# Performance work log

Measured on AMD Instinct MI355X. Metric: run time of the kernel, lower is better.

Reference implementation:

```python
import jax, jax.numpy as jnp
import numpy as np

# Standard SMPL kinematic tree (parent of each of the 24 joints)
PARENTS = np.array([-1, 0, 0, 0, 1, 2, 3, 4, 5, 6, 7, 8, 9, 9, 9, 12, 13, 14, 16, 17, 18, 19, 20, 21])
B, V, NJ = 512, 6890, 24


def rodrigues(r):
    # r: (N,3) axis-angle -> (N,3,3) rotation matrices
    theta = jnp.linalg.norm(r, axis=1, keepdims=True) + 1e-8  # (N,1), eps mirrors the noise trick in torch code
    rh = r / theta                                            # (N,3) unit axis
    x, y, z = rh[:, 0], rh[:, 1], rh[:, 2]
    zero = jnp.zeros_like(x)
    K = jnp.stack([zero, -z, y, z, zero, -x, -y, x, zero], axis=1).reshape(-1, 3, 3)
    cos = jnp.cos(theta)[:, :, None]
    sin = jnp.sin(theta)[:, :, None]
    outer = rh[:, :, None] * rh[:, None, :]
    I3 = jnp.eye(3, dtype=r.dtype)
    return cos * I3 + (1.0 - cos) * outer + sin * K


def _make_A(Ri, ti):
    # Ri: (B,3,3), ti: (B,3) -> homogeneous (B,4,4)
    Rt = jnp.concatenate([Ri, ti[:, :, None]], axis=2)  # (B,3,4)
    bottom = jnp.broadcast_to(jnp.array([0.0, 0.0, 0.0, 1.0], dtype=Ri.dtype), (Ri.shape[0], 1, 4))
    return jnp.concatenate([Rt, bottom], axis=1)


def smpl_forward(betas, pose, trans, v_template, shapedirs, posedirs, J_regressor, joint_regressor, weights):
    b = betas.shape[0]
    # shape blend shapes
    v_shaped = jnp.einsum('bs,vcs->bvc', betas, shapedirs) + v_template  # (B,V,3)
    J = jnp.einsum('jv,bvc->bjc', J_regressor, v_shaped)                 # (B,24,3)
    R = rodrigues(pose.reshape(-1, 3)).reshape(b, NJ, 3, 3)              # (B,24,3,3)
    I3 = jnp.eye(3, dtype=pose.dtype)
    lrotmin = (R[:, 1:] - I3).reshape(b, (NJ - 1) * 9)                   # (B,207)
    v_posed = v_shaped + jnp.einsum('bp,vcp->bvc', lrotmin, posedirs)    # pose blend shapes
    # forward kinematics along the chain (fixed 24-joint loop)
    Gs = [_make_A(R[:, 0], J[:, 0])]
    for i in range(1, NJ):
        p = int(PARENTS[i])
        Gs.append(jnp.matmul(Gs[p], _make_A(R[:, i], J[:, i] - J[:, p])))
    G = jnp.stack(Gs, axis=1)                                            # (B,24,4,4)
    # remove rest-pose joint locations (the 'pack' subtraction)
    Jh = jnp.concatenate([J, jnp.zeros((b, NJ, 1), dtype=J.dtype)], axis=2)  # (B,24,4)
    t = jnp.einsum('bjxy,bjy->bjx', G, Jh)                               # (B,24,4)
    G = G - jnp.pad(t[..., None], ((0, 0), (0, 0), (0, 0), (3, 0)))      # subtract in last column
    # linear blend skinning
    T = jnp.einsum('bjxy,vj->bvxy', G, weights)                          # (B,V,4,4) -- large, memory bound
    vh = jnp.concatenate([v_posed, jnp.ones((b, v_posed.shape[1], 1), dtype=v_posed.dtype)], axis=2)
    v = jnp.einsum('bvxy,bvy->bvx', T, vh)[..., :3]                      # (B,V,3)
    result = v + trans[:, None, :]
    joints = jnp.einsum('bvc,jv->bjc', result, joint_regressor)          # (B,24,3)
    return result, joints


def setup_inputs() -> dict:
    key = jax.random.key(0)
    ks = jax.random.split(key, 9)
    betas = jax.random.normal(ks[0], (B, 10), dtype=jnp.float32)
    pose = jax.random.normal(ks[1], (B, 72), dtype=jnp.float32) * 0.3
    trans = jax.random.normal(ks[2], (B, 3), dtype=jnp.float32)
    v_template = jax.random.normal(ks[3], (V, 3), dtype=jnp.float32) * 0.3
    shapedirs = jax.random.normal(ks[4], (V, 3, 10), dtype=jnp.float32) * 0.01
    posedirs = jax.random.normal(ks[5], (V, 3, 207), dtype=jnp.float32) * 0.01
    Jr = jax.random.uniform(ks[6], (NJ, V), dtype=jnp.float32)
    J_regressor = Jr / jnp.sum(Jr, axis=1, keepdims=True)
    jr2 = jax.random.uniform(ks[7], (NJ, V), dtype=jnp.float32)
    joint_regressor = jr2 / jnp.sum(jr2, axis=1, keepdims=True)
    w = jax.random.uniform(ks[8], (V, NJ), dtype=jnp.float32)
    weights = w / jnp.sum(w, axis=1, keepdims=True)
    return {"betas": betas, "pose": pose, "trans": trans, "v_template": v_template,
            "shapedirs": shapedirs, "posedirs": posedirs, "J_regressor": J_regressor,
            "joint_regressor": joint_regressor, "weights": weights}


def reference(betas, pose, trans, v_template, shapedirs, posedirs, J_regressor, joint_regressor, weights):
    return smpl_forward(betas, pose, trans, v_template, shapedirs, posedirs, J_regressor, joint_regressor, weights)
```

## Files before the change

kernel.cpp:

```cpp
#include <hip/hip_runtime.h>
#include <hip/hip_bf16.h>

#define VNUM 6890
#define VPAD 6912
#define BNUM 512
#define NJ 24

typedef short bf16x8 __attribute__((ext_vector_type(8)));
typedef float f32x4 __attribute__((ext_vector_type(4)));

__device__ __forceinline__ short f2bf(float x) {
    union { float f; unsigned u; } v; v.f = x;
    unsigned r = v.u + 0x7fff + ((v.u >> 16) & 1);
    return (short)(r >> 16);
}

#define WS_JS 0
#define WS_LWX 800
#define WS_GA 58144
#define WS_WT 156448
#define WS_PB 267040
#define WS_PART 267040

#define RES_ELEMS (512 * 6890 * 3)

__global__ __launch_bounds__(256) void ka_kernel(const float* __restrict__ Jr,
                                                 const float* __restrict__ sd,
                                                 const float* __restrict__ vt,
                                                 float* __restrict__ part) {
    int j = blockIdx.x;
    int ch = blockIdx.y;
    int tid = threadIdx.x;
    int vbeg = ch * 864;
    int vend = min(vbeg + 864, VNUM);
    float acc[33];
#pragma unroll
    for (int k = 0; k < 33; ++k) acc[k] = 0.f;
    for (int v = vbeg + tid; v < vend; v += 256) {
        float q = Jr[j * VNUM + v];
#pragma unroll
        for (int c = 0; c < 3; ++c) {
#pragma unroll
            for (int s = 0; s < 10; ++s)
                acc[c * 11 + s] += q * sd[v * 30 + c * 10 + s];
            acc[c * 11 + 10] += q * vt[v * 3 + c];
        }
    }
#pragma unroll
    for (int k = 0; k < 33; ++k) {
        float a = acc[k];
#pragma unroll
        for (int off = 32; off >= 1; off >>= 1) a += __shfl_xor(a, off);
        acc[k] = a;
    }
    __shared__ float red[4][33];
    int lane = tid & 63, wid = tid >> 6;
    if (lane == 0) {
#pragma unroll
        for (int k = 0; k < 33; ++k) red[wid][k] = acc[k];
    }
    __syncthreads();
    if (tid < 33)
        part[(j * 8 + ch) * 33 + tid] = red[0][tid] + red[1][tid] + red[2][tid] + red[3][tid];
}

__global__ __launch_bounds__(64) void ka2_kernel(const float* __restrict__ part,
                                                 float* __restrict__ js) {
    int j = blockIdx.x;
    int t = threadIdx.x;
    if (t < 33) {
        float a = 0.f;
#pragma unroll
        for (int ch = 0; ch < 8; ++ch) a += part[(j * 8 + ch) * 33 + t];
        js[j * 33 + t] = a;
    }
}

__global__ __launch_bounds__(64) void kb_kernel(const float* __restrict__ pose,
                                                const float* __restrict__ betas,
                                                const float* __restrict__ trans,
                                                const float* __restrict__ js,
                                                short* __restrict__ lwX,
                                                short* __restrict__ ga) {
    int b = blockIdx.x;
    int t = threadIdx.x;
    __shared__ float Rl[24][9];
    __shared__ float Jl[24][3];
    __shared__ float Gl[24][12];

    if (t < 24) {
        float x = pose[b * 72 + t * 3 + 0];
        float y = pose[b * 72 + t * 3 + 1];
        float z = pose[b * 72 + t * 3 + 2];
        float th = sqrtf(x * x + y * y + z * z) + 1e-8f;
        float rx = x / th, ry = y / th, rz = z / th;
        float cs = cosf(th), sn = sinf(th), mc = 1.f - cs;
        float R[9];
        R[0] = cs + mc * rx * rx;      R[1] = mc * rx * ry - sn * rz; R[2] = mc * rx * rz + sn * ry;
        R[3] = mc * ry * rx + sn * rz; R[4] = cs + mc * ry * ry;      R[5] = mc * ry * rz - sn * rx;
        R[6] = mc * rz * rx - sn * ry; R[7] = mc * rz * ry + sn * rx; R[8] = cs + mc * rz * rz;
#pragma unroll
        for (int k = 0; k < 9; ++k) Rl[t][k] = R[k];
        if (t >= 1) {
#pragma unroll
            for (int k = 0; k < 9; ++k)
                lwX[b * 224 + (t - 1) * 9 + k] =
                    f2bf(R[k] - ((k == 0 || k == 4 || k == 8) ? 1.f : 0.f));
        }
#pragma unroll
        for (int c = 0; c < 3; ++c) {
            float a = js[(t * 3 + c) * 11 + 10];
#pragma unroll
            for (int s = 0; s < 10; ++s) a += betas[b * 10 + s] * js[(t * 3 + c) * 11 + s];
            Jl[t][c] = a;
        }
    } else if (t >= 32 && t < 42) {
        lwX[b * 224 + 207 + (t - 32)] = f2bf(betas[b * 10 + (t - 32)]);
    } else if (t == 42) {
        lwX[b * 224 + 217] = f2bf(1.f);
    } else if (t >= 43 && t < 49) {
        lwX[b * 224 + 218 + (t - 43)] = 0;
    }
    __syncthreads();

    if (t < 12) {
        int x = t >> 2, yy = t & 3;
        Gl[0][t] = (yy < 3) ? Rl[0][x * 3 + yy] : Jl[0][x];
    }
    __syncthreads();

    const int par[24] = {-1, 0, 0, 0, 1, 2, 3, 4, 5, 6, 7, 8, 9, 9, 9, 12, 13, 14, 16, 17, 18, 19, 20, 21};
#pragma unroll
    for (int i = 1; i < 24; ++i) {
        if (t < 12) {
            int x = t >> 2, yy = t & 3;
            int p = par[i];
            float a0, a1, a2, add;
            if (yy < 3) {
                a0 = Rl[i][0 * 3 + yy]; a1 = Rl[i][1 * 3 + yy]; a2 = Rl[i][2 * 3 + yy]; add = 0.f;
            } else {
                a0 = Jl[i][0] - Jl[p][0]; a1 = Jl[i][1] - Jl[p][1]; a2 = Jl[i][2] - Jl[p][2];
                add = Gl[p][x * 4 + 3];
            }
            Gl[i][t] = Gl[p][x * 4 + 0] * a0 + Gl[p][x * 4 + 1] * a1 + Gl[p][x * 4 + 2] * a2 + add;
        }
        __syncthreads();
    }

    if (t < 24) {
#pragma unroll
        for (int x = 0; x < 3; ++x) {
            float tx = Gl[t][x * 4 + 0] * Jl[t][0] + Gl[t][x * 4 + 1] * Jl[t][1] + Gl[t][x * 4 + 2] * Jl[t][2];
#pragma unroll
            for (int yy = 0; yy < 3; ++yy)
                ga[(x * 4 + yy) * (512 * 32) + b * 32 + t] = f2bf(Gl[t][x * 4 + yy]);
            ga[(x * 4 + 3) * (512 * 32) + b * 32 + t] =
                f2bf(Gl[t][x * 4 + 3] - tx + trans[b * 3 + x]);
        }
    } else if (t < 32) {
#pragma unroll
        for (int r = 0; r < 12; ++r) ga[r * (512 * 32) + b * 32 + t] = 0;
    }
}

__global__ __launch_bounds__(256) void pe_kernel(const float* __restrict__ pd,
                                                 const float* __restrict__ sd,
                                                 const float* __restrict__ vt,
                                                 short* __restrict__ pb) {
    int v0 = blockIdx.x * 32;
    int c = blockIdx.y;
    int t = threadIdx.x;
    int vloc = t >> 3, sub = t & 7;
    int v = v0 + vloc;
    short* dst = pb + ((size_t)c * VPAD + v) * 224;
    if (v < VNUM) {
        const float* pr = pd + (size_t)v * 621 + c * 207;
        const float* sr = sd + (size_t)v * 30 + c * 10;
        float vtv = vt[v * 3 + c];
#pragma unroll
        for (int i = 0; i < 28; ++i) {
            int k = sub + i * 8;
            float val;
            if (k < 207) val = pr[k];
            else if (k < 217) val = sr[k - 207];
            else if (k == 217) val = vtv;
            else val = 0.f;
            dst[k] = f2bf(val);
        }
    } else {
#pragma unroll
        for (int i = 0; i < 28; ++i) dst[sub + i * 8] = 0;
    }
}

__global__ __launch_bounds__(256) void wp_kernel(const float* __restrict__ w,
                                                 short* __restrict__ wt) {
    int v = blockIdx.x * 256 + threadIdx.x;
    if (v >= VPAD) return;
    short* dst = wt + (size_t)v * 32;
    if (v < VNUM) {
#pragma unroll
        for (int j = 0; j < 24; ++j) dst[j] = f2bf(w[(size_t)v * 24 + j]);
#pragma unroll
        for (int j = 24; j < 32; ++j) dst[j] = 0;
    } else {
#pragma unroll
        for (int j = 0; j < 32; ++j) dst[j] = 0;
    }
}

__global__ __launch_bounds__(256) void km_kernel(const short* __restrict__ lwX,
                                                 const short* __restrict__ pb,
                                                 const short* __restrict__ ga,
                                                 const short* __restrict__ wt,
                                                 float* __restrict__ out) {
    int d = blockIdx.x;
    int xcd = d & 7;
    int q = d >> 3;
    int by = (q >> 4) * 8 + xcd;
    int bx = q & 15;
    if (by >= 54) return;

    int tid = threadIdx.x;
    int lane = tid & 63;
    int wid = tid >> 6;
    int row = lane & 15;
    int kq = lane >> 4;
    int b0 = bx * 32;
    int v0 = by * 128 + wid * 32;

    f32x4 vp[2][2][3];
#pragma unroll
    for (int m = 0; m < 2; ++m)
#pragma unroll
        for (int vb = 0; vb < 2; ++vb)
#pragma unroll
            for (int c = 0; c < 3; ++c) vp[m][vb][c] = (f32x4){0.f, 0.f, 0.f, 0.f};

    const short* arow0 = lwX + (b0 + row) * 224 + kq * 8;
    const short* arow1 = arow0 + 16 * 224;
#pragma unroll
    for (int ks = 0; ks < 7; ++ks) {
        bf16x8 a0 = *(const bf16x8*)(arow0 + ks * 32);
        bf16x8 a1 = *(const bf16x8*)(arow1 + ks * 32);
#pragma unroll
        for (int vb = 0; vb < 2; ++vb) {
#pragma unroll
            for (int c = 0; c < 3; ++c) {
                bf16x8 bf = *(const bf16x8*)(pb + ((size_t)c * VPAD + v0 + vb * 16 + row) * 224 +
                                             ks * 32 + kq * 8);
                vp[0][vb][c] = __builtin_amdgcn_mfma_f32_16x16x32_bf16(a0, bf, vp[0][vb][c], 0, 0, 0);
                vp[1][vb][c] = __builtin_amdgcn_mfma_f32_16x16x32_bf16(a1, bf, vp[1][vb][c], 0, 0, 0);
            }
        }
    }

    bf16x8 wfrag[2];
#pragma unroll
    for (int vb = 0; vb < 2; ++vb)
        wfrag[vb] = *(const bf16x8*)(wt + (size_t)(v0 + vb * 16 + row) * 32 + kq * 8);

    const f32x4 zero4 = {0.f, 0.f, 0.f, 0.f};
    int brow = kq * 4;

    float resAll[2][2][4][3];

#pragma unroll
    for (int x = 0; x < 3; ++x) {
        f32x4 res[2][2];
        {
            int r = x * 4 + 3;
            bf16x8 g0 = *(const bf16x8*)(ga + ((size_t)r * 512 + b0 + row) * 32 + kq * 8);
            bf16x8 g1 = *(const bf16x8*)(ga + ((size_t)r * 512 + b0 + 16 + row) * 32 + kq * 8);
#pragma unroll
            for (int vb = 0; vb < 2; ++vb) {
                res[0][vb] = __builtin_amdgcn_mfma_f32_16x16x32_bf16(g0, wfrag[vb], zero4, 0, 0, 0);
                res[1][vb] = __builtin_amdgcn_mfma_f32_16x16x32_bf16(g1, wfrag[vb], zero4, 0, 0, 0);
            }
        }
#pragma unroll
        for (int y = 0; y < 3; ++y) {
            int r = x * 4 + y;
            bf16x8 g0 = *(const bf16x8*)(ga + ((size_t)r * 512 + b0 + row) * 32 + kq * 8);
            bf16x8 g1 = *(const bf16x8*)(ga + ((size_t)r * 512 + b0 + 16 + row) * 32 + kq * 8);
#pragma unroll
            for (int vb = 0; vb < 2; ++vb) {
                f32x4 t0 = __builtin_amdgcn_mfma_f32_16x16x32_bf16(g0, wfrag[vb], zero4, 0, 0, 0);
                f32x4 t1 = __builtin_amdgcn_mfma_f32_16x16x32_bf16(g1, wfrag[vb], zero4, 0, 0, 0);
#pragma unroll
                for (int reg = 0; reg < 4; ++reg) {
                    res[0][vb][reg] += t0[reg] * vp[0][vb][y][reg];
                    res[1][vb][reg] += t1[reg] * vp[1][vb][y][reg];
                }
            }
        }
#pragma unroll
        for (int m = 0; m < 2; ++m)
#pragma unroll
            for (int vb = 0; vb < 2; ++vb)
#pragma unroll
                for (int reg = 0; reg < 4; ++reg)
                    resAll[m][vb][reg][x] = res[m][vb][reg];
    }

#pragma unroll
    for (int m = 0; m < 2; ++m) {
#pragma unroll
        for (int vb = 0; vb < 2; ++vb) {
            int v = v0 + vb * 16 + row;
            if (v < VNUM) {
#pragma unroll
                for (int reg = 0; reg < 4; ++reg) {
                    int b = b0 + m * 16 + brow + reg;
                    float* op = out + ((size_t)b * VNUM + v) * 3;
                    op[0] = resAll[m][vb][reg][0];
                    op[1] = resAll[m][vb][reg][1];
                    op[2] = resAll[m][vb][reg][2];
                }
            }
        }
    }
}

__global__ __launch_bounds__(256) void kd_kernel(const float* __restrict__ res,
                                                 const float* __restrict__ jr2,
                                                 float* __restrict__ joints) {
    int d = blockIdx.x;
    int vq = d & 7;
    int b = d >> 3;
    int tid = threadIdx.x;
    int lane = tid & 63;
    int w = tid >> 6;
    int j0 = w * 6;
    int vbeg = vq * 864;
    int vend = min(vbeg + 864, VNUM);

    float acc[6][3];
#pragma unroll
    for (int jj = 0; jj < 6; ++jj)
#pragma unroll
        for (int c = 0; c < 3; ++c) acc[jj][c] = 0.f;

    const float* rb = res + (size_t)b * VNUM * 3;
    for (int v = vbeg + lane; v < vend; v += 64) {
        float r0 = rb[v * 3 + 0];
        float r1 = rb[v * 3 + 1];
        float r2 = rb[v * 3 + 2];
#pragma unroll
        for (int jj = 0; jj < 6; ++jj) {
            float q = jr2[(size_t)(j0 + jj) * VNUM + v];
            acc[jj][0] += q * r0;
            acc[jj][1] += q * r1;
            acc[jj][2] += q * r2;
        }
    }

#pragma unroll
    for (int jj = 0; jj < 6; ++jj)
#pragma unroll
        for (int c = 0; c < 3; ++c) {
            float a = acc[jj][c];
#pragma unroll
            for (int off = 32; off >= 1; off >>= 1) a += __shfl_xor(a, off);
            if (lane == 0)
                atomicAdd(&joints[(size_t)b * 72 + (j0 + jj) * 3 + c], a);
        }
}

extern "C" void kernel_launch(void* const* d_in, const int* in_sizes, int n_in,
                              void* d_out, int out_size, void* d_ws, size_t ws_size,
                              hipStream_t stream) {
    const float* betas = (const float*)d_in[0];
    const float* pose = (const float*)d_in[1];
    const float* trans = (const float*)d_in[2];
    const float* v_template = (const float*)d_in[3];
    const float* shapedirs = (const float*)d_in[4];
    const float* posedirs = (const float*)d_in[5];
    const float* J_regressor = (const float*)d_in[6];
    const float* joint_regressor = (const float*)d_in[7];
    const float* weights = (const float*)d_in[8];
    float* out = (float*)d_out;

    float* wsf = (float*)d_ws;
    float* js = wsf + WS_JS;
    float* part = wsf + WS_PART;
    short* lwX = (short*)(wsf + WS_LWX);
    short* ga = (short*)(wsf + WS_GA);
    short* wt = (short*)(wsf + WS_WT);
    short* pb = (short*)(wsf + WS_PB);

    hipMemsetAsync((void*)(out + RES_ELEMS), 0, (size_t)512 * 72 * 4, stream);

    ka_kernel<<<dim3(24, 8), 256, 0, stream>>>(J_regressor, shapedirs, v_template, part);
    ka2_kernel<<<24, 64, 0, stream>>>(part, js);
    pe_kernel<<<dim3(216, 3), 256, 0, stream>>>(posedirs, shapedirs, v_template, pb);
    wp_kernel<<<27, 256, 0, stream>>>(weights, wt);
    kb_kernel<<<512, 64, 0, stream>>>(pose, betas, trans, js, lwX, ga);
    km_kernel<<<896, 256, 0, stream>>>(lwX, pb, ga, wt, out);
    kd_kernel<<<4096, 256, 0, stream>>>(out, joint_regressor, out + RES_ELEMS);
}
```

Baseline: 113.5 us.

## Tile joint-regressor reduction through LDS and reuse across eight batches

New measurement: 225.8 us. 98.9% more time.

```diff
diff --git a/kernel.cpp b/kernel.cpp
--- a/kernel.cpp
+++ b/kernel.cpp
@@ -5,6 +5,9 @@
 #define VPAD 6912
 #define BNUM 512
 #define NJ 24
+
+#define KD_CH 320
+#define KD_NCH 22
 
 typedef short bf16x8 __attribute__((ext_vector_type(8)));
 typedef float f32x4 __attribute__((ext_vector_type(4)));
@@ -325,46 +328,69 @@
 __global__ __launch_bounds__(256) void kd_kernel(const float* __restrict__ res,
                                                  const float* __restrict__ jr2,
                                                  float* __restrict__ joints) {
+    __shared__ float jl[24][KD_CH];
+    __shared__ float rl[KD_CH * 3];
+
     int d = blockIdx.x;
-    int vq = d & 7;
-    int b = d >> 3;
+    int ch = d % KD_NCH;
+    int bg = d / KD_NCH;
+    int b0 = bg * 8;
+    int vbeg = ch * KD_CH;
     int tid = threadIdx.x;
     int lane = tid & 63;
     int w = tid >> 6;
     int j0 = w * 6;
-    int vbeg = vq * 864;
-    int vend = min(vbeg + 864, VNUM);
-
-    float acc[6][3];
-#pragma unroll
-    for (int jj = 0; jj < 6; ++jj)
-#pragma unroll
-        for (int c = 0; c < 3; ++c) acc[jj][c] = 0.f;
-
-    const float* rb = res + (size_t)b * VNUM * 3;
-    for (int v = vbeg + lane; v < vend; v += 64) {
-        float r0 = rb[v * 3 + 0];
-        float r1 = rb[v * 3 + 1];
-        float r2 = rb[v * 3 + 2];
-#pragma unroll
-        for (int jj = 0; jj < 6; ++jj) {
-            float q = jr2[(size_t)(j0 + jj) * VNUM + v];
-            acc[jj][0] += q * r0;
-            acc[jj][1] += q * r1;
-            acc[jj][2] += q * r2;
-        }
-    }
-
-#pragma unroll
-    for (int jj = 0; jj < 6; ++jj)
-#pragma unroll
-        for (int c = 0; c < 3; ++c) {
-            float a = acc[jj][c];
-#pragma unroll
-            for (int off = 32; off >= 1; off >>= 1) a += __shfl_xor(a, off);
-            if (lane == 0)
-                atomicAdd(&joints[(size_t)b * 72 + (j0 + jj) * 3 + c], a);
-        }
+
+    for (int idx = tid; idx < 24 * KD_CH; idx += 256) {
+        int j = idx / KD_CH;
+        int vl = idx - j * KD_CH;
+        int v = vbeg + vl;
+        jl[j][vl] = (v < VNUM) ? jr2[(size_t)j * VNUM + v] : 0.f;
+    }
+
+    for (int bb = 0; bb < 8; ++bb) {
+        int b = b0 + bb;
+        const float* rb = res + (size_t)b * VNUM * 3;
+        __syncthreads();
+        int base = vbeg * 3;
+        for (int idx = tid; idx < KD_CH * 3; idx += 256) {
+            int g = base + idx;
+            rl[idx] = (g < VNUM * 3) ? rb[g] : 0.f;
+        }
+        __syncthreads();
+
+        float acc[6][3];
+#pragma unroll
+        for (int jj = 0; jj < 6; ++jj)
+#pragma unroll
+            for (int c = 0; c < 3; ++c) acc[jj][c] = 0.f;
+
+#pragma unroll
+        for (int it = 0; it < KD_CH / 64; ++it) {
+            int vl = it * 64 + lane;
+            float r0 = rl[vl * 3 + 0];
+            float r1 = rl[vl * 3 + 1];
+            float r2 = rl[vl * 3 + 2];
+#pragma unroll
+            for (int jj = 0; jj < 6; ++jj) {
+                float qv = jl[j0 + jj][vl];
+                acc[jj][0] = fmaf(qv, r0, acc[jj][0]);
+                acc[jj][1] = fmaf(qv, r1, acc[jj][1]);
+                acc[jj][2] = fmaf(qv, r2, acc[jj][2]);
+            }
+        }
+
+#pragma unroll
+        for (int jj = 0; jj < 6; ++jj)
+#pragma unroll
+            for (int c = 0; c < 3; ++c) {
+                float a = acc[jj][c];
+#pragma unroll
+                for (int off = 32; off >= 1; off >>= 1) a += __shfl_xor(a, off);
+                if (lane == 0)
+                    atomicAdd(&joints[(size_t)b * 72 + (j0 + jj) * 3 + c], a);
+            }
+    }
 }
 
 extern "C" void kernel_launch(void* const* d_in, const int* in_sizes, int n_in,
@@ -397,5 +423,5 @@
     wp_kernel<<<27, 256, 0, stream>>>(weights, wt);
     kb_kernel<<<512, 64, 0, stream>>>(pose, betas, trans, js, lwX, ga);
     km_kernel<<<896, 256, 0, stream>>>(lwX, pb, ga, wt, out);
-    kd_kernel<<<4096, 256, 0, stream>>>(out, joint_regressor, out + RES_ELEMS);
-}
+    kd_kernel<<<1408, 256, 0, stream>>>(out, joint_regressor, out + RES_ELEMS);
+}
```

## Compute joint regression with bf16 MFMA after transposing vertices

Applied to the files above, without the earlier changes.

Result: slower. 119.2 us (+5.0%).

```diff
diff --git a/kernel.cpp b/kernel.cpp
--- a/kernel.cpp
+++ b/kernel.cpp
@@ -21,6 +21,9 @@
 #define WS_WT 156448
 #define WS_PB 267040
 #define WS_PART 267040
+#define WS_REST 2589472
+#define WS_JR2B 7897888
+#define WS_NEED_BYTES ((size_t)8008480 * 4)
 
 #define RES_ELEMS (512 * 6890 * 3)
 
@@ -322,6 +325,83 @@
     }
 }
 
+__global__ __launch_bounds__(256) void jq_kernel(const float* __restrict__ jr2,
+                                                 short* __restrict__ jr2b) {
+    int j = blockIdx.x;
+    for (int v = threadIdx.x; v < VPAD; v += 256) {
+        float val = (j < NJ && v < VNUM) ? jr2[(size_t)j * VNUM + v] : 0.f;
+        jr2b[(size_t)j * VPAD + v] = f2bf(val);
+    }
+}
+
+__global__ __launch_bounds__(256) void kt_kernel(const float* __restrict__ res,
+                                                 unsigned short* __restrict__ resT) {
+    __shared__ unsigned short lt[3][256];
+    int v0 = blockIdx.x * 256;
+    int b = blockIdx.y;
+    int tid = threadIdx.x;
+    int v = v0 + tid;
+    float r0 = 0.f, r1 = 0.f, r2 = 0.f;
+    if (v < VNUM) {
+        const float* p = res + ((size_t)b * VNUM + v) * 3;
+        r0 = p[0]; r1 = p[1]; r2 = p[2];
+    }
+    lt[0][tid] = (unsigned short)f2bf(r0);
+    lt[1][tid] = (unsigned short)f2bf(r1);
+    lt[2][tid] = (unsigned short)f2bf(r2);
+    __syncthreads();
+    for (int k = tid; k < 3 * 128; k += 256) {
+        int c = k >> 7, u = k & 127;
+        unsigned int val = (unsigned int)lt[c][2 * u] | ((unsigned int)lt[c][2 * u + 1] << 16);
+        *(unsigned int*)&resT[((size_t)b * 3 + c) * VPAD + v0 + 2 * u] = val;
+    }
+}
+
+__global__ __launch_bounds__(256) void kj_kernel(const short* __restrict__ jr2b,
+                                                 const short* __restrict__ resT,
+                                                 float* __restrict__ joints) {
+    __shared__ float Lc[4][32][17];
+    int n0 = blockIdx.x * 16;
+    int tid = threadIdx.x;
+    int lane = tid & 63;
+    int w = tid >> 6;
+    int row = lane & 15;
+    int kq = lane >> 4;
+
+    f32x4 acc[2];
+    acc[0] = (f32x4){0.f, 0.f, 0.f, 0.f};
+    acc[1] = (f32x4){0.f, 0.f, 0.f, 0.f};
+
+    const short* arow0 = jr2b + (size_t)row * VPAD + kq * 8;
+    const short* arow1 = arow0 + 16 * VPAD;
+    const short* brow = resT + (size_t)(n0 + row) * VPAD + kq * 8;
+
+    int ks0 = w * 54, ks1 = ks0 + 54;
+    for (int ks = ks0; ks < ks1; ++ks) {
+        bf16x8 a0 = *(const bf16x8*)(arow0 + ks * 32);
+        bf16x8 a1 = *(const bf16x8*)(arow1 + ks * 32);
+        bf16x8 bf = *(const bf16x8*)(brow + ks * 32);
+        acc[0] = __builtin_amdgcn_mfma_f32_16x16x32_bf16(a0, bf, acc[0], 0, 0, 0);
+        acc[1] = __builtin_amdgcn_mfma_f32_16x16x32_bf16(a1, bf, acc[1], 0, 0, 0);
+    }
+
+#pragma unroll
+    for (int m = 0; m < 2; ++m)
+#pragma unroll
+        for (int reg = 0; reg < 4; ++reg)
+            Lc[w][m * 16 + kq * 4 + reg][row] = acc[m][reg];
+    __syncthreads();
+
+    for (int idx = tid; idx < 32 * 16; idx += 256) {
+        int j = idx >> 4, n = idx & 15;
+        if (j < NJ) {
+            float s = Lc[0][j][n] + Lc[1][j][n] + Lc[2][j][n] + Lc[3][j][n];
+            int nn = n0 + n;
+            joints[(size_t)(nn / 3) * 72 + j * 3 + (nn % 3)] = s;
+        }
+    }
+}
+
 __global__ __launch_bounds__(256) void kd_kernel(const float* __restrict__ res,
                                                  const float* __restrict__ jr2,
                                                  float* __restrict__ joints) {
@@ -388,6 +468,10 @@
     short* ga = (short*)(wsf + WS_GA);
     short* wt = (short*)(wsf + WS_WT);
     short* pb = (short*)(wsf + WS_PB);
+    unsigned short* resT = (unsigned short*)(wsf + WS_REST);
+    short* jr2b = (short*)(wsf + WS_JR2B);
+
+    bool big = ws_size >= WS_NEED_BYTES;
 
     hipMemsetAsync((void*)(out + RES_ELEMS), 0, (size_t)512 * 72 * 4, stream);
 
@@ -396,6 +480,12 @@
     pe_kernel<<<dim3(216, 3), 256, 0, stream>>>(posedirs, shapedirs, v_template, pb);
     wp_kernel<<<27, 256, 0, stream>>>(weights, wt);
     kb_kernel<<<512, 64, 0, stream>>>(pose, betas, trans, js, lwX, ga);
+    if (big) jq_kernel<<<32, 256, 0, stream>>>(joint_regressor, jr2b);
     km_kernel<<<896, 256, 0, stream>>>(lwX, pb, ga, wt, out);
-    kd_kernel<<<4096, 256, 0, stream>>>(out, joint_regressor, out + RES_ELEMS);
-}
+    if (big) {
+        kt_kernel<<<dim3(27, 512), 256, 0, stream>>>(out, resT);
+        kj_kernel<<<96, 256, 0, stream>>>(jr2b, (const short*)resT, out + RES_ELEMS);
+    } else {
+        kd_kernel<<<4096, 256, 0, stream>>>(out, joint_regressor, out + RES_ELEMS);
+    }
+}
```
